# Performance work log

Measured on AMD Instinct MI355X. Metric: run time of the kernel, lower is better.

The kernel has to match this reference:

```python
import jax, jax.numpy as jnp
import numpy as np

N_NODES = 50000
N_EDGES = 800000
FEAT_DIM = 64
NUM_RELS = 8


def setup_inputs() -> dict:
    key = jax.random.key(0)
    k1, k2, k3, k4, k5 = jax.random.split(key, 5)
    features = jax.random.normal(k1, (N_NODES, FEAT_DIM), dtype=jnp.float32)
    # xavier_uniform with relu gain ~= sqrt(2)*sqrt(6/(D+D))
    limit = np.sqrt(2.0) * np.sqrt(6.0 / (FEAT_DIM + FEAT_DIM))
    weight_r = jax.random.uniform(k2, (NUM_RELS, FEAT_DIM, FEAT_DIM), dtype=jnp.float32,
                                  minval=-limit, maxval=limit)
    src = jax.random.randint(k3, (N_EDGES,), 0, N_NODES, dtype=jnp.int64 if jax.config.jax_enable_x64 else jnp.int32)
    dst = jax.random.randint(k4, (N_EDGES,), 0, N_NODES, dtype=src.dtype)
    etype = jax.random.randint(k5, (N_EDGES,), 0, NUM_RELS, dtype=src.dtype)
    return {"features": features, "weight_r": weight_r, "src": src, "dst": dst, "etype": etype}


def reference(features, weight_r, src, dst, etype):
    N, D = features.shape
    c = 0.2
    # in-degree of each destination node (DGL 'deg' node data)
    deg = jax.ops.segment_sum(jnp.ones(dst.shape, dtype=features.dtype), dst, num_segments=N)
    # relation-batched matmul: h @ W_r for every relation, then gather per edge.
    # [R, N, D] = 8*50000*64 floats -- cheap vs. materializing [E, D, D] weights.
    hw = jnp.einsum('nd,rdf->rnf', features, weight_r)
    msg = hw[etype, src] / deg[dst][:, None]          # [E, D]
    M = jax.ops.segment_sum(msg, dst, num_segments=N)  # scatter-sum mailbox reduce
    updated = jax.nn.relu(c * features + (1.0 - c) * M)
    # DGL only applies reduce to nodes that received messages; others keep h.
    return jnp.where((deg > 0)[:, None], updated, features)
```

## Files before the change

kernel.cpp:

```cpp
#include <hip/hip_runtime.h>
#include <hip/hip_bf16.h>

#define N_NODES 50000
#define N_EDGES 800000
#define FEAT 64
#define NRELS 8
#define NSUP 196
#define SCAP 5120
#define NBP 196
#define RIDERS 196
#define NPB 32
#define NBUCK 1563
#define BCAP 768

typedef __attribute__((ext_vector_type(8))) short bf16x8;
typedef __attribute__((ext_vector_type(4))) float f32x4;

static __host__ __device__ inline size_t align256(size_t x) { return (x + 255) & ~(size_t)255; }

__device__ inline unsigned short f2b(float f) {
    unsigned u = __builtin_bit_cast(unsigned, f);
    unsigned r = (u + 0x7fffu + ((u >> 16) & 1u)) >> 16;
    return (unsigned short)r;
}
__device__ inline float b2f(unsigned short u) {
    unsigned v = ((unsigned)u) << 16;
    return __builtin_bit_cast(float, v);
}

__global__ void bfill_kernel(const int* __restrict__ dst, const int* __restrict__ srcv,
                             const int* __restrict__ et,
                             int* __restrict__ tmp, int* __restrict__ cnts,
                             int E) {
    __shared__ int pkL[4096];
    __shared__ int hist[NSUP];
    __shared__ int lbase[NSUP];
    __shared__ int lcur[NSUP];
    __shared__ int wsum[4];
    __shared__ int totS;
    const int t = threadIdx.x;
    const int blk = blockIdx.x;

    for (int j = t; j < NSUP; j += 256) hist[j] = 0;
    __syncthreads();

    const int4* dst4 = (const int4*)dst;
    const int4* src4 = (const int4*)srcv;
    const int4* et4  = (const int4*)et;
    const int n4 = E >> 2;
    int sup[16], pk[16];
#pragma unroll
    for (int k = 0; k < 4; k++) {
        int i4 = blk * 1024 + t + k * 256;
        if (i4 < n4) {
            int4 d = dst4[i4];
            int4 s = src4[i4];
            int4 r = et4[i4];
            const int dd[4] = {d.x, d.y, d.z, d.w};
            const int ss[4] = {s.x, s.y, s.z, s.w};
            const int rr[4] = {r.x, r.y, r.z, r.w};
#pragma unroll
            for (int j = 0; j < 4; j++) {
                int idx = k * 4 + j;
                sup[idx] = dd[j] >> 8;
                pk[idx] = (ss[j] & 0xFFFF) | (rr[j] << 16) | ((dd[j] & 255) << 19);
                atomicAdd(&hist[sup[idx]], 1);
            }
        } else {
#pragma unroll
            for (int j = 0; j < 4; j++) sup[k * 4 + j] = -1;
        }
    }
    __syncthreads();

    const int myc = (t < NSUP) ? hist[t] : 0;
    int x = myc;
#pragma unroll
    for (int o = 1; o < 64; o <<= 1) {
        int u_ = __shfl_up(x, o);
        if ((t & 63) >= o) x += u_;
    }
    if ((t & 63) == 63) wsum[t >> 6] = x;
    __syncthreads();
    {
        int add = 0;
        const int wv = t >> 6;
        if (wv > 0) add += wsum[0];
        if (wv > 1) add += wsum[1];
        if (wv > 2) add += wsum[2];
        x += add;
    }
    const int ex = x - myc;
    if (t < NSUP) {
        lbase[t] = ex;
        lcur[t] = ex;
        cnts[t * NBP + blk] = (ex << 16) | myc;
    }
    if (t == 255) totS = x;
    __syncthreads();

#pragma unroll
    for (int k = 0; k < 16; k++) {
        if (sup[k] >= 0) {
            int p = atomicAdd(&lcur[sup[k]], 1);
            pkL[p] = pk[k];
        }
    }
    __syncthreads();

    const int total = totS;
    int* seg = tmp + (size_t)blk * 4096;
    for (int i = t; i < total; i += 256) seg[i] = pkL[i];
}

__global__ __launch_bounds__(1024, 1) void sortk_kernel(
    const int* __restrict__ tmp, const int* __restrict__ cnts,
    int* __restrict__ spk, int* __restrict__ off_s, int* __restrict__ off_e,
    const float* __restrict__ W, const float* __restrict__ feat,
    unsigned short* __restrict__ WtT, unsigned short* __restrict__ Fb, int N) {
    __shared__ int pkL[SCAP];
    __shared__ int sorted_[SCAP];
    __shared__ int hist2[2048];
    __shared__ int runB[NBP];
    __shared__ int runS[NBP];
    __shared__ int runC[NBP];
    __shared__ int wsum[16];
    __shared__ int totEs;
    const int t = threadIdx.x;

    if (blockIdx.x >= NSUP) {
        const int fbb = blockIdx.x - NSUP;
        if (fbb < 8) {
            int i4 = fbb * 1024 + t;
            float4 v = ((const float4*)W)[i4];
            int bse = i4 * 4;
            int f0 = bse & 63;
            int rd = bse >> 6;
            int d  = rd & 63;
            int r  = rd >> 6;
            unsigned short* w0 = WtT + ((size_t)(r * 64 + f0) * 64 + d);
            w0[0 * 64] = f2b(v.x);
            w0[1 * 64] = f2b(v.y);
            w0[2 * 64] = f2b(v.z);
            w0[3 * 64] = f2b(v.w);
        }
        const int node = fbb * 256 + (t >> 2);
        if (node >= N) return;
        const int seg = t & 3;
        const float4* F4 = (const float4*)feat + (size_t)node * 16 + seg * 4;
        float4 v0 = F4[0], v1 = F4[1], v2 = F4[2], v3 = F4[3];
        bf16x8 b0, b1;
        b0[0] = (short)f2b(v0.x); b0[1] = (short)f2b(v0.y);
        b0[2] = (short)f2b(v0.z); b0[3] = (short)f2b(v0.w);
        b0[4] = (short)f2b(v1.x); b0[5] = (short)f2b(v1.y);
        b0[6] = (short)f2b(v1.z); b0[7] = (short)f2b(v1.w);
        b1[0] = (short)f2b(v2.x); b1[1] = (short)f2b(v2.y);
        b1[2] = (short)f2b(v2.z); b1[3] = (short)f2b(v2.w);
        b1[4] = (short)f2b(v3.x); b1[5] = (short)f2b(v3.y);
        b1[6] = (short)f2b(v3.z); b1[7] = (short)f2b(v3.w);
        *(bf16x8*)(Fb + (size_t)node * 64 + seg * 16)     = b0;
        *(bf16x8*)(Fb + (size_t)node * 64 + seg * 16 + 8) = b1;
        return;
    }
    const int s = blockIdx.x;

    if (t < NBP) {
        int pc = cnts[s * NBP + t];
        runS[t] = pc >> 16;
        runC[t] = pc & 0xFFFF;
    }
    __syncthreads();
    if (t < 256) {
        const int myc = (t < NBP) ? runC[t] : 0;
        int x = myc;
#pragma unroll
        for (int o = 1; o < 64; o <<= 1) {
            int u_ = __shfl_up(x, o);
            if ((t & 63) >= o) x += u_;
        }
        if ((t & 63) == 63) wsum[t >> 6] = x;
        __syncthreads();
        int add = 0;
        const int wv = t >> 6;
        if (wv > 0) add += wsum[0];
        if (wv > 1) add += wsum[1];
        if (wv > 2) add += wsum[2];
        x += add;
        if (t < NBP) runB[t] = x - myc;
        if (t == 255) totEs = min(x, SCAP);
    } else {
        __syncthreads();
    }
    __syncthreads();
    const int totE = totEs;

    {
        const int w = t >> 6, lane = t & 63;
        for (int r = w; r < NBP; r += 16) {
            const int c = runC[r];
            const int bse = runB[r];
            const int* srcp = tmp + (size_t)r * 4096 + runS[r];
            for (int i = lane; i < c; i += 64) {
                int o = bse + i;
                if (o < SCAP) pkL[o] = srcp[i];
            }
        }
    }
    hist2[t] = 0;
    hist2[t + 1024] = 0;
    __syncthreads();

    for (int i = t; i < totE; i += 1024) {
        int v = pkL[i];
        atomicAdd(&hist2[(((v >> 19) & 255) << 3) | ((v >> 16) & 7)], 1);
    }
    __syncthreads();
    const int loc0 = hist2[2 * t], loc1 = hist2[2 * t + 1];
    {
        const int T = loc0 + loc1;
        int x = T;
#pragma unroll
        for (int o = 1; o < 64; o <<= 1) {
            int u_ = __shfl_up(x, o);
            if ((t & 63) >= o) x += u_;
        }
        if ((t & 63) == 63) wsum[t >> 6] = x;
        __syncthreads();
        int add = 0;
        const int wv = t >> 6;
#pragma unroll
        for (int v_ = 0; v_ < 16; v_++) if (v_ < wv) add += wsum[v_];
        x += add;
        hist2[2 * t]     = x - T;
        hist2[2 * t + 1] = x - T + loc0;
    }
    __syncthreads();
    if (t < 256) {
        const int gn = s * 256 + t;
        if (gn < N) {
            const int st = hist2[8 * t];
            const int en = (t == 255) ? totE : hist2[8 * t + 8];
            off_s[gn] = s * SCAP + st;
            off_e[gn] = s * SCAP + en;
        }
    }
    __syncthreads();
    for (int i = t; i < totE; i += 1024) {
        int v = pkL[i];
        int pos = atomicAdd(&hist2[(((v >> 19) & 255) << 3) | ((v >> 16) & 7)], 1);
        if (pos < SCAP) sorted_[pos] = v;
    }
    __syncthreads();
    for (int i = t; i < totE; i += 1024) spk[(size_t)s * SCAP + i] = sorted_[i];
}

__global__ __launch_bounds__(256, 4) void fuse_kernel(
    const int* __restrict__ spk, const int* __restrict__ off_s,
    const int* __restrict__ off_e, const unsigned short* __restrict__ Fb,
    const unsigned short* __restrict__ WtT, const float* __restrict__ feat,
    float* __restrict__ out, int N) {
    __shared__ unsigned short Sb[NRELS][NPB][64];
    __shared__ int sedge[BCAP];
    const int t = threadIdx.x;
    const int bkt = blockIdx.x;
    const int n0 = bkt * NPB;
    const int nn = min(NPB, N - n0);
    const int gid = t >> 3, q = t & 7;

    {
        f32x4 z = {0.f, 0.f, 0.f, 0.f};
        f32x4* zp = (f32x4*)&Sb[0][0][0];
#pragma unroll
        for (int i = 0; i < 8; i++) zp[t + 256 * i] = z;
    }

    const int b0 = off_s[n0];
    const int eL = off_e[n0 + nn - 1];
    for (int i = b0 + t; i < eL; i += 256) {
        int o = i - b0;
        if (o < BCAP) sedge[o] = spk[i];
    }
    __syncthreads();

    int b = 0, e = 0, deg = 0;
    if (gid < nn) {
        const int rb = off_s[n0 + gid], re = off_e[n0 + gid];
        deg = re - rb;
        b = rb - b0;
        e = min(re - b0, BCAP);
    }
    if (gid < nn && b < e) {
        const int swz = (q ^ (gid & 7)) * 8;
        unsigned short* srow = &Sb[0][0][0] + (size_t)gid * 64 + swz;
        float a[8] = {0.f, 0.f, 0.f, 0.f, 0.f, 0.f, 0.f, 0.f};
        int curR = -1;

        auto flushS = [&](int rel) {
            bf16x8 v;
#pragma unroll
            for (int k = 0; k < 8; k++) v[k] = (short)f2b(a[k]);
            *(bf16x8*)(srow + (size_t)rel * (NPB * 64)) = v;
        };
        auto issue = [&](int cb, int (&pk)[8], bf16x8 (&u)[8]) {
#pragma unroll
            for (int j = 0; j < 8; j++) {
                int p = (cb + j < e) ? sedge[cb + j] : -1;
                pk[j] = p;
                if (p >= 0)
                    u[j] = *(const bf16x8*)(Fb + (size_t)(p & 0xFFFF) * 64 + q * 8);
            }
        };
        auto consume = [&](int (&pk)[8], bf16x8 (&u)[8]) {
#pragma unroll
            for (int j = 0; j < 8; j++) {
                int p = pk[j];
                if (p >= 0) {
                    bf16x8 uu = u[j];
                    int rel = (p >> 16) & 7;
                    if (rel != curR) {
                        if (curR >= 0) flushS(curR);
                        curR = rel;
#pragma unroll
                        for (int k = 0; k < 8; k++) a[k] = b2f((unsigned short)uu[k]);
                    } else {
#pragma unroll
                        for (int k = 0; k < 8; k++) a[k] += b2f((unsigned short)uu[k]);
                    }
                }
            }
        };

        bf16x8 z8 = {0, 0, 0, 0, 0, 0, 0, 0};
        int pkA[8] = {-1, -1, -1, -1, -1, -1, -1, -1};
        int pkB[8] = {-1, -1, -1, -1, -1, -1, -1, -1};
        bf16x8 uA[8] = {z8, z8, z8, z8, z8, z8, z8, z8};
        bf16x8 uB[8] = {z8, z8, z8, z8, z8, z8, z8, z8};

        issue(b, pkA, uA);
        __builtin_amdgcn_sched_barrier(0);
#pragma unroll
        for (int c = 0; c < 4; c++) {
            const int nb = b + (c + 1) * 8;
            if ((c & 1) == 0) {
                if (c < 3 && nb < e) issue(nb, pkB, uB);
                __builtin_amdgcn_sched_barrier(0);
                consume(pkA, uA);
            } else {
                if (c < 3 && nb < e) issue(nb, pkA, uA);
                __builtin_amdgcn_sched_barrier(0);
                consume(pkB, uB);
            }
            if (nb >= e) break;
        }
        for (int i = b + 32; i < e; i++) {
            int p = sedge[i];
            bf16x8 uu = *(const bf16x8*)(Fb + (size_t)(p & 0xFFFF) * 64 + q * 8);
            int rel = (p >> 16) & 7;
            if (rel != curR) {
                if (curR >= 0) flushS(curR);
                curR = rel;
#pragma unroll
                for (int k = 0; k < 8; k++) a[k] = b2f((unsigned short)uu[k]);
            } else {
#pragma unroll
                for (int k = 0; k < 8; k++) a[k] += b2f((unsigned short)uu[k]);
            }
        }
        if (curR >= 0) flushS(curR);
    }

    float4 h0e = make_float4(0.f, 0.f, 0.f, 0.f), h1e = h0e;
    const int ef0 = q * 8;
    if (gid < nn) {
        const float4* fp = (const float4*)feat + (size_t)(n0 + gid) * 16 + (ef0 >> 2);
        h0e = fp[0];
        h1e = fp[1];
    }
    __syncthreads();

    const int w = t >> 6, l = t & 63, col = l & 15, quad = l >> 4;
    f32x4 acc0 = {0.f, 0.f, 0.f, 0.f}, acc1 = {0.f, 0.f, 0.f, 0.f};
    const int sw0 = (quad ^ (col & 7)) * 8;
    const int sw1 = ((quad + 4) ^ (col & 7)) * 8;
#pragma unroll
    for (int r = 0; r < NRELS; r++) {
        const unsigned short* wp = WtT + (size_t)r * 4096 + ((w * 16 + col) * 64 + quad * 8);
        bf16x8 b0 = *(const bf16x8*)wp;
        bf16x8 b1 = *(const bf16x8*)(wp + 32);
        const unsigned short* Sr = &Sb[0][0][0] + (size_t)r * (NPB * 64);
        bf16x8 a0 = *(const bf16x8*)&Sr[col * 64 + sw0];
        bf16x8 a1 = *(const bf16x8*)&Sr[col * 64 + sw1];
        bf16x8 c0 = *(const bf16x8*)&Sr[(16 + col) * 64 + sw0];
        bf16x8 c1 = *(const bf16x8*)&Sr[(16 + col) * 64 + sw1];
        acc0 = __builtin_amdgcn_mfma_f32_16x16x32_bf16(a0, b0, acc0, 0, 0, 0);
        acc0 = __builtin_amdgcn_mfma_f32_16x16x32_bf16(a1, b1, acc0, 0, 0, 0);
        acc1 = __builtin_amdgcn_mfma_f32_16x16x32_bf16(c0, b0, acc1, 0, 0, 0);
        acc1 = __builtin_amdgcn_mfma_f32_16x16x32_bf16(c1, b1, acc1, 0, 0, 0);
    }
    __syncthreads();

    float* C = (float*)&Sb[0][0][0];
#pragma unroll
    for (int i = 0; i < 4; i++) {
        C[(quad * 4 + i) * 72 + w * 16 + col]        = acc0[i];
        C[(16 + quad * 4 + i) * 72 + w * 16 + col]   = acc1[i];
    }
    __syncthreads();

    if (gid < nn) {
        const int gn = n0 + gid;
        float4 m0 = *(const float4*)&C[gid * 72 + ef0];
        float4 m1 = *(const float4*)&C[gid * 72 + ef0 + 4];
        float4 r0, r1;
        if (deg > 0) {
            float inv = 0.8f / (float)deg;
            r0.x = fmaxf(0.2f * h0e.x + m0.x * inv, 0.f);
            r0.y = fmaxf(0.2f * h0e.y + m0.y * inv, 0.f);
            r0.z = fmaxf(0.2f * h0e.z + m0.z * inv, 0.f);
            r0.w = fmaxf(0.2f * h0e.w + m0.w * inv, 0.f);
            r1.x = fmaxf(0.2f * h1e.x + m1.x * inv, 0.f);
            r1.y = fmaxf(0.2f * h1e.y + m1.y * inv, 0.f);
            r1.z = fmaxf(0.2f * h1e.z + m1.z * inv, 0.f);
            r1.w = fmaxf(0.2f * h1e.w + m1.w * inv, 0.f);
        } else {
            r0 = h0e; r1 = h1e;
        }
        float4* op = (float4*)out + (size_t)gn * 16 + (ef0 >> 2);
        op[0] = r0;
        op[1] = r1;
    }
}

__global__ void degf_kernel(const int* __restrict__ dst, float* __restrict__ deg, int E) {
    int e = blockIdx.x * blockDim.x + threadIdx.x;
    if (e < E) atomicAdd(deg + dst[e], 1.0f);
}

__global__ void otf_kernel(const int* __restrict__ src, const int* __restrict__ dst,
                           const int* __restrict__ et, const float* __restrict__ feat,
                           const float* __restrict__ W, float* __restrict__ out, int E) {
    int wid = (blockIdx.x * blockDim.x + threadIdx.x) >> 6;
    int l = threadIdx.x & 63;
    if (wid >= E) return;
    int s = src[wid], dd = dst[wid], r = et[wid];
    float fv = feat[(size_t)s * 64 + l];
    const float* Wr = W + (size_t)r * 4096;
    float acc = 0.f;
#pragma unroll
    for (int d = 0; d < 64; d++) {
        float a = __shfl(fv, d);
        acc += a * Wr[d * 64 + l];
    }
    atomicAdd(out + (size_t)dd * 64 + l, acc);
}

__global__ void final_kernel(const float* __restrict__ feat, const float* __restrict__ deg,
                             float* __restrict__ out, int N) {
    int i = blockIdx.x * blockDim.x + threadIdx.x;
    if (i >= N * 16) return;
    int n = i >> 4;
    float d = deg[n];
    float4 f = ((const float4*)feat)[i];
    float4 m = ((float4*)out)[i];
    float4 res;
    if (d > 0.f) {
        float inv = 0.8f / d;
        res.x = fmaxf(0.2f * f.x + m.x * inv, 0.f);
        res.y = fmaxf(0.2f * f.y + m.y * inv, 0.f);
        res.z = fmaxf(0.2f * f.z + m.z * inv, 0.f);
        res.w = fmaxf(0.2f * f.w + m.w * inv, 0.f);
    } else {
        res = f;
    }
    ((float4*)out)[i] = res;
}

extern "C" void kernel_launch(void* const* d_in, const int* in_sizes, int n_in,
                              void* d_out, int out_size, void* d_ws, size_t ws_size,
                              hipStream_t stream) {
    const float* feat = (const float*)d_in[0];
    const float* W    = (const float*)d_in[1];
    const int*   src  = (const int*)d_in[2];
    const int*   dst  = (const int*)d_in[3];
    const int*   et   = (const int*)d_in[4];
    float* out = (float*)d_out;

    const int N = N_NODES, E = N_EDGES;

    char* p = (char*)d_ws;
    int* tmp   = (int*)p;  p += align256((size_t)NBP * 4096 * 4);
    int* cnts  = (int*)p;  p += align256((size_t)NSUP * NBP * 4);
    int* spk   = (int*)p;  p += align256((size_t)NSUP * SCAP * 4);
    int* off_s = (int*)p;  p += align256((size_t)N * 4);
    int* off_e = (int*)p;  p += align256((size_t)N * 4);
    unsigned short* WtT = (unsigned short*)p;
    p += align256((size_t)NRELS * FEAT * FEAT * 2);
    unsigned short* Fb = (unsigned short*)p;
    p += align256((size_t)N * FEAT * 2);
    size_t need_full = (size_t)(p - (char*)d_ws);

    if (ws_size >= need_full) {
        bfill_kernel<<<NBP, 256, 0, stream>>>(dst, src, et, tmp, cnts, E);
        sortk_kernel<<<NSUP + RIDERS, 1024, 0, stream>>>(tmp, cnts, spk, off_s, off_e,
                                                         W, feat, WtT, Fb, N);
        fuse_kernel<<<NBUCK, 256, 0, stream>>>(spk, off_s, off_e, Fb, WtT,
                                               feat, out, N);
    } else {
        float* deg = (float*)d_ws;
        hipMemsetAsync(out, 0, (size_t)N * FEAT * 4, stream);
        hipMemsetAsync(deg, 0, (size_t)N * 4, stream);
        degf_kernel<<<(E + 255) / 256, 256, 0, stream>>>(dst, deg, E);
        otf_kernel<<<(E + 3) / 4, 256, 0, stream>>>(src, dst, et, feat, W, out, E);
        final_kernel<<<(N * 16 + 255) / 256, 256, 0, stream>>>(feat, deg, out, N);
    }
}
```

Before: 126.3 us.

## Split each node's edge list across two thread groups and halve nodes per block

Halves nodes per fuse block (32 to 16), doubling the block count, and assigns two 8-lane groups per destination node, each aggregating half of the relation-sorted edge list, using a new midpoint offset array written by the sort kernel at relation 4. The MFMA stage drops to one 16-row tile per wave, and the epilogue writes one float4 per thread. The intent is more parallelism and occupancy for the gather-heavy aggregation, with shorter per-thread edge chains. In exchange it adds an extra offset array and shared-memory offset loads, a shallower prefetch pipeline, and it assumes N is a multiple of 16 since the tail-node guards are removed.

After: 150.0 us. 1.19x slower.

```diff
diff --git a/kernel.cpp b/kernel.cpp
--- a/kernel.cpp
+++ b/kernel.cpp
@@ -9,9 +9,9 @@
 #define SCAP 5120
 #define NBP 196
 #define RIDERS 196
-#define NPB 32
-#define NBUCK 1563
-#define BCAP 768
+#define NPB 16
+#define NBUCK 3125
+#define BCAP 512
 
 typedef __attribute__((ext_vector_type(8))) short bf16x8;
 typedef __attribute__((ext_vector_type(4))) float f32x4;
@@ -115,7 +115,8 @@
 
 __global__ __launch_bounds__(1024, 1) void sortk_kernel(
     const int* __restrict__ tmp, const int* __restrict__ cnts,
-    int* __restrict__ spk, int* __restrict__ off_s, int* __restrict__ off_e,
+    int* __restrict__ spk, int* __restrict__ off_s, int* __restrict__ off_m,
+    int* __restrict__ off_e,
     const float* __restrict__ W, const float* __restrict__ feat,
     unsigned short* __restrict__ WtT, unsigned short* __restrict__ Fb, int N) {
     __shared__ int pkL[SCAP];
@@ -239,8 +240,10 @@
         const int gn = s * 256 + t;
         if (gn < N) {
             const int st = hist2[8 * t];
+            const int md = hist2[8 * t + 4];
             const int en = (t == 255) ? totE : hist2[8 * t + 8];
             off_s[gn] = s * SCAP + st;
+            off_m[gn] = s * SCAP + md;
             off_e[gn] = s * SCAP + en;
         }
     }
@@ -254,44 +257,47 @@
     for (int i = t; i < totE; i += 1024) spk[(size_t)s * SCAP + i] = sorted_[i];
 }
 
-__global__ __launch_bounds__(256, 4) void fuse_kernel(
+__global__ __launch_bounds__(256, 6) void fuse_kernel(
     const int* __restrict__ spk, const int* __restrict__ off_s,
-    const int* __restrict__ off_e, const unsigned short* __restrict__ Fb,
+    const int* __restrict__ off_m, const int* __restrict__ off_e,
+    const unsigned short* __restrict__ Fb,
     const unsigned short* __restrict__ WtT, const float* __restrict__ feat,
     float* __restrict__ out, int N) {
     __shared__ unsigned short Sb[NRELS][NPB][64];
     __shared__ int sedge[BCAP];
+    __shared__ int nofS[NPB], nofM[NPB], nofE[NPB];
     const int t = threadIdx.x;
     const int bkt = blockIdx.x;
     const int n0 = bkt * NPB;
-    const int nn = min(NPB, N - n0);
     const int gid = t >> 3, q = t & 7;
+    const int node = gid >> 1, h = gid & 1;
 
     {
         f32x4 z = {0.f, 0.f, 0.f, 0.f};
         f32x4* zp = (f32x4*)&Sb[0][0][0];
 #pragma unroll
-        for (int i = 0; i < 8; i++) zp[t + 256 * i] = z;
-    }
-
-    const int b0 = off_s[n0];
-    const int eL = off_e[n0 + nn - 1];
+        for (int i = 0; i < 4; i++) zp[t + 256 * i] = z;
+    }
+    if (t < NPB) {
+        nofS[t] = off_s[n0 + t];
+        nofM[t] = off_m[n0 + t];
+        nofE[t] = off_e[n0 + t];
+    }
+    __syncthreads();
+
+    const int b0 = nofS[0];
+    const int eL = nofE[NPB - 1];
     for (int i = b0 + t; i < eL; i += 256) {
         int o = i - b0;
         if (o < BCAP) sedge[o] = spk[i];
     }
     __syncthreads();
 
-    int b = 0, e = 0, deg = 0;
-    if (gid < nn) {
-        const int rb = off_s[n0 + gid], re = off_e[n0 + gid];
-        deg = re - rb;
-        b = rb - b0;
-        e = min(re - b0, BCAP);
-    }
-    if (gid < nn && b < e) {
-        const int swz = (q ^ (gid & 7)) * 8;
-        unsigned short* srow = &Sb[0][0][0] + (size_t)gid * 64 + swz;
+    int b = min((h ? nofM[node] : nofS[node]) - b0, BCAP);
+    int e = min((h ? nofE[node] : nofM[node]) - b0, BCAP);
+    if (b < e) {
+        const int swz = (q ^ (node & 7)) * 8;
+        unsigned short* srow = &Sb[0][0][0] + (size_t)node * 64 + swz;
         float a[8] = {0.f, 0.f, 0.f, 0.f, 0.f, 0.f, 0.f, 0.f};
         int curR = -1;
 
@@ -338,21 +344,11 @@
 
         issue(b, pkA, uA);
         __builtin_amdgcn_sched_barrier(0);
-#pragma unroll
-        for (int c = 0; c < 4; c++) {
-            const int nb = b + (c + 1) * 8;
-            if ((c & 1) == 0) {
-                if (c < 3 && nb < e) issue(nb, pkB, uB);
-                __builtin_amdgcn_sched_barrier(0);
-                consume(pkA, uA);
-            } else {
-                if (c < 3 && nb < e) issue(nb, pkA, uA);
-                __builtin_amdgcn_sched_barrier(0);
-                consume(pkB, uB);
-            }
-            if (nb >= e) break;
-        }
-        for (int i = b + 32; i < e; i++) {
+        if (b + 8 < e) issue(b + 8, pkB, uB);
+        __builtin_amdgcn_sched_barrier(0);
+        consume(pkA, uA);
+        if (b + 8 < e) consume(pkB, uB);
+        for (int i = b + 16; i < e; i++) {
             int p = sedge[i];
             bf16x8 uu = *(const bf16x8*)(Fb + (size_t)(p & 0xFFFF) * 64 + q * 8);
             int rel = (p >> 16) & 7;
@@ -369,17 +365,16 @@
         if (curR >= 0) flushS(curR);
     }
 
-    float4 h0e = make_float4(0.f, 0.f, 0.f, 0.f), h1e = h0e;
-    const int ef0 = q * 8;
-    if (gid < nn) {
-        const float4* fp = (const float4*)feat + (size_t)(n0 + gid) * 16 + (ef0 >> 2);
-        h0e = fp[0];
-        h1e = fp[1];
+    const int en_ = t >> 4, ef_ = t & 15;
+    float4 hfe;
+    {
+        const float4* fp = (const float4*)feat + (size_t)(n0 + en_) * 16 + ef_;
+        hfe = fp[0];
     }
     __syncthreads();
 
     const int w = t >> 6, l = t & 63, col = l & 15, quad = l >> 4;
-    f32x4 acc0 = {0.f, 0.f, 0.f, 0.f}, acc1 = {0.f, 0.f, 0.f, 0.f};
+    f32x4 acc0 = {0.f, 0.f, 0.f, 0.f};
     const int sw0 = (quad ^ (col & 7)) * 8;
     const int sw1 = ((quad + 4) ^ (col & 7)) * 8;
 #pragma unroll
@@ -390,44 +385,32 @@
         const unsigned short* Sr = &Sb[0][0][0] + (size_t)r * (NPB * 64);
         bf16x8 a0 = *(const bf16x8*)&Sr[col * 64 + sw0];
         bf16x8 a1 = *(const bf16x8*)&Sr[col * 64 + sw1];
-        bf16x8 c0 = *(const bf16x8*)&Sr[(16 + col) * 64 + sw0];
-        bf16x8 c1 = *(const bf16x8*)&Sr[(16 + col) * 64 + sw1];
         acc0 = __builtin_amdgcn_mfma_f32_16x16x32_bf16(a0, b0, acc0, 0, 0, 0);
         acc0 = __builtin_amdgcn_mfma_f32_16x16x32_bf16(a1, b1, acc0, 0, 0, 0);
-        acc1 = __builtin_amdgcn_mfma_f32_16x16x32_bf16(c0, b0, acc1, 0, 0, 0);
-        acc1 = __builtin_amdgcn_mfma_f32_16x16x32_bf16(c1, b1, acc1, 0, 0, 0);
     }
     __syncthreads();
 
     float* C = (float*)&Sb[0][0][0];
 #pragma unroll
-    for (int i = 0; i < 4; i++) {
-        C[(quad * 4 + i) * 72 + w * 16 + col]        = acc0[i];
-        C[(16 + quad * 4 + i) * 72 + w * 16 + col]   = acc1[i];
-    }
-    __syncthreads();
-
-    if (gid < nn) {
-        const int gn = n0 + gid;
-        float4 m0 = *(const float4*)&C[gid * 72 + ef0];
-        float4 m1 = *(const float4*)&C[gid * 72 + ef0 + 4];
-        float4 r0, r1;
+    for (int i = 0; i < 4; i++)
+        C[(quad * 4 + i) * 72 + w * 16 + col] = acc0[i];
+    __syncthreads();
+
+    {
+        const int gn = n0 + en_;
+        const int deg = nofE[en_] - nofS[en_];
+        float4 m = *(const float4*)&C[en_ * 72 + ef_ * 4];
+        float4 r0;
         if (deg > 0) {
             float inv = 0.8f / (float)deg;
-            r0.x = fmaxf(0.2f * h0e.x + m0.x * inv, 0.f);
-            r0.y = fmaxf(0.2f * h0e.y + m0.y * inv, 0.f);
-            r0.z = fmaxf(0.2f * h0e.z + m0.z * inv, 0.f);
-            r0.w = fmaxf(0.2f * h0e.w + m0.w * inv, 0.f);
-            r1.x = fmaxf(0.2f * h1e.x + m1.x * inv, 0.f);
-            r1.y = fmaxf(0.2f * h1e.y + m1.y * inv, 0.f);
-            r1.z = fmaxf(0.2f * h1e.z + m1.z * inv, 0.f);
-            r1.w = fmaxf(0.2f * h1e.w + m1.w * inv, 0.f);
+            r0.x = fmaxf(0.2f * hfe.x + m.x * inv, 0.f);
+            r0.y = fmaxf(0.2f * hfe.y + m.y * inv, 0.f);
+            r0.z = fmaxf(0.2f * hfe.z + m.z * inv, 0.f);
+            r0.w = fmaxf(0.2f * hfe.w + m.w * inv, 0.f);
         } else {
-            r0 = h0e; r1 = h1e;
-        }
-        float4* op = (float4*)out + (size_t)gn * 16 + (ef0 >> 2);
-        op[0] = r0;
-        op[1] = r1;
+            r0 = hfe;
+        }
+        ((float4*)out)[(size_t)gn * 16 + ef_] = r0;
     }
 }
 
@@ -492,6 +475,7 @@
     int* cnts  = (int*)p;  p += align256((size_t)NSUP * NBP * 4);
     int* spk   = (int*)p;  p += align256((size_t)NSUP * SCAP * 4);
     int* off_s = (int*)p;  p += align256((size_t)N * 4);
+    int* off_m = (int*)p;  p += align256((size_t)N * 4);
     int* off_e = (int*)p;  p += align256((size_t)N * 4);
     unsigned short* WtT = (unsigned short*)p;
     p += align256((size_t)NRELS * FEAT * FEAT * 2);
@@ -501,10 +485,11 @@
 
     if (ws_size >= need_full) {
         bfill_kernel<<<NBP, 256, 0, stream>>>(dst, src, et, tmp, cnts, E);
-        sortk_kernel<<<NSUP + RIDERS, 1024, 0, stream>>>(tmp, cnts, spk, off_s, off_e,
+        sortk_kernel<<<NSUP + RIDERS, 1024, 0, stream>>>(tmp, cnts, spk,
+                                                         off_s, off_m, off_e,
                                                          W, feat, WtT, Fb, N);
-        fuse_kernel<<<NBUCK, 256, 0, stream>>>(spk, off_s, off_e, Fb, WtT,
-                                               feat, out, N);
+        fuse_kernel<<<NBUCK, 256, 0, stream>>>(spk, off_s, off_m, off_e,
+                                               Fb, WtT, feat, out, N);
     } else {
         float* deg = (float*)d_ws;
         hipMemsetAsync(out, 0, (size_t)N * FEAT * 4, stream);
```
